# Kernel optimization log

Measured on AMD Instinct MI355X. Metric: run time of the kernel, lower is better.

## Reference

```python
import jax, jax.numpy as jnp
import numpy as np

N_NODES = 100000
N_EDGES = 1600000
N_FEAT = 128
HID = 64
HEADS = 3
CHROM = 21
N_CLASSES = 10
N_GRAPHS = 8
NEG_SLOPE = 0.2
EPS = 1e-5


def _glorot(key, shape):
    fan_in, fan_out = shape[0], shape[-1]
    lim = float(np.sqrt(6.0 / (fan_in + fan_out)))
    return jax.random.uniform(key, shape, jnp.float32, -lim, lim)


def setup_inputs() -> dict:
    key = jax.random.key(0)
    ks = jax.random.split(key, 16)
    x = jax.random.normal(ks[0], (N_NODES, N_FEAT), jnp.float32)
    src = jax.random.randint(ks[1], (N_EDGES,), 0, N_NODES)
    dst = jax.random.randint(ks[2], (N_EDGES,), 0, N_NODES)
    # avoid pre-existing self loops (PyG removes them before adding fresh ones)
    dst = jnp.where(dst == src, (dst + 1) % N_NODES, dst)
    edge_index = jnp.stack([src, dst]).astype(jnp.int64)
    batch = jnp.sort(jax.random.randint(ks[3], (N_NODES,), 0, N_GRAPHS)).astype(jnp.int64)
    d1 = HEADS * HID
    params = {
        # conv1: in 128 -> heads*64, concat=True
        'Wl1': _glorot(ks[4], (N_FEAT, d1)), 'Wr1': _glorot(ks[5], (N_FEAT, d1)),
        'att1': _glorot(ks[6], (HEADS, HID)), 'b1': jnp.zeros((d1,), jnp.float32),
        # batchnorm over 192 features
        'gamma': jnp.ones((d1,), jnp.float32), 'beta': jnp.zeros((d1,), jnp.float32),
        # conv2: in 192 -> 64 (mean over heads)
        'Wl2': _glorot(ks[7], (d1, d1)), 'Wr2': _glorot(ks[8], (d1, d1)),
        'att2': _glorot(ks[9], (HEADS, HID)), 'b2': jnp.zeros((HID,), jnp.float32),
        # conv3: in 64 -> 21 (mean over heads)
        'Wl3': _glorot(ks[10], (HID, HEADS * CHROM)), 'Wr3': _glorot(ks[11], (HID, HEADS * CHROM)),
        'att3': _glorot(ks[12], (HEADS, CHROM)), 'b3': jnp.zeros((CHROM,), jnp.float32),
        # classifier (sized to actual conv2 output width = HID)
        'Wc': _glorot(ks[13], (HID, N_CLASSES)), 'bc': jnp.zeros((N_CLASSES,), jnp.float32),
    }
    return {'x': x, 'edge_index': edge_index, 'batch': batch, **params}


def gatv2(x, src, dst, Wl, Wr, att, bias, concat):
    N = x.shape[0]
    H, D = att.shape
    xl = (x @ Wl).reshape(N, H, D)   # source transform (messages)
    xr = (x @ Wr).reshape(N, H, D)   # target transform
    e = jax.nn.leaky_relu(xl[src] + xr[dst], NEG_SLOPE)          # [E,H,D]
    logits = jnp.einsum('ehd,hd->eh', e, att)                    # [E,H]
    m = jax.ops.segment_max(logits, dst, num_segments=N)         # segment softmax over incoming edges
    ez = jnp.exp(logits - m[dst])
    z = jax.ops.segment_sum(ez, dst, num_segments=N)
    alpha = ez / z[dst]                                          # [E,H]; self-loops guarantee nonempty segments
    out = jax.ops.segment_sum(xl[src] * alpha[:, :, None], dst, num_segments=N)  # [N,H,D]
    out = out.reshape(N, H * D) if concat else out.mean(axis=1)
    return out + bias


def batchnorm(x, gamma, beta):
    mu = x.mean(axis=0)
    var = x.var(axis=0)
    return (x - mu) * jax.lax.rsqrt(var + EPS) * gamma + beta


def reference(x, edge_index, batch, Wl1, Wr1, att1, b1, gamma, beta,
              Wl2, Wr2, att2, b2, Wl3, Wr3, att3, b3, Wc, bc):
    N = x.shape[0]
    loop = jnp.arange(N, dtype=edge_index.dtype)
    src = jnp.concatenate([edge_index[0], loop])
    dst = jnp.concatenate([edge_index[1], loop])

    h = gatv2(x, src, dst, Wl1, Wr1, att1, b1, concat=True)      # [N, 192]
    h = jax.nn.relu(h)
    h = batchnorm(h, gamma, beta)
    h = gatv2(h, src, dst, Wl2, Wr2, att2, b2, concat=False)     # [N, 64]
    color = jax.nn.relu(h)
    color = gatv2(color, src, dst, Wl3, Wr3, att3, b3, concat=False)  # [N, 21]

    # global mean pool over graphs (dropout is eval-mode identity)
    sums = jax.ops.segment_sum(h, batch, num_segments=N_GRAPHS)
    cnt = jax.ops.segment_sum(jnp.ones((N, 1), h.dtype), batch, num_segments=N_GRAPHS)
    pooled = sums / jnp.maximum(cnt, 1.0)                        # [8, 64]
    classif = pooled @ Wc + bc                                   # [8, 10]
    return classif, color
```

## Files before the change

kernel.cpp:

```cpp
#include <hip/hip_runtime.h>
#include <stdint.h>
#include <math.h>

#define N_NODES 100000
#define N_EDGES 1600000
#define ETOT (N_EDGES + N_NODES)
#define NCLS 10
#define NGR 8
#define SCAN_BLOCKS ((N_NODES + 255) / 256)

typedef short v8s __attribute__((ext_vector_type(8)));
typedef float v4f __attribute__((ext_vector_type(4)));
typedef float f4v __attribute__((ext_vector_type(4)));
typedef unsigned short ushort_t;
typedef unsigned short us8 __attribute__((ext_vector_type(8)));
typedef unsigned short us4 __attribute__((ext_vector_type(4)));
typedef _Float16 h2 __attribute__((ext_vector_type(2)));
typedef _Float16 h4 __attribute__((ext_vector_type(4)));
typedef _Float16 h8 __attribute__((ext_vector_type(8)));

__device__ __forceinline__ float b2f(ushort_t u) {
    union { unsigned int i; float f; } v; v.i = ((unsigned int)u) << 16; return v.f;
}
__device__ __forceinline__ ushort_t f2b(float f) {
    union { float f; unsigned int i; } v; v.f = f;
    unsigned int u = v.i;
    unsigned int r = (u + 0x7fffu + ((u >> 16) & 1u)) >> 16;
    return (ushort_t)r;
}
__device__ __forceinline__ ushort_t f2h(float f) {
    union { _Float16 h; ushort_t u; } v; v.h = (_Float16)f; return v.u;
}

#if __has_builtin(__builtin_amdgcn_fdot2)
#define FDOT2(a, b, c) __builtin_amdgcn_fdot2((a), (b), (c), false)
#else
#define FDOT2(a, b, c) ((c) + (float)(a)[0] * (float)(b)[0] + (float)(a)[1] * (float)(b)[1])
#endif
#define SHUF2(v, i, j) __builtin_shufflevector((v), (v), (i), (j))

__device__ __forceinline__ h2 lrelu2(h2 t) {
    const h2 k = {(_Float16)0.2f, (_Float16)0.2f};
    return __builtin_elementwise_max(t, t * k);
}

__global__ void detect_kernel(const int* eidx, const unsigned int* gamma_raw,
                              int* nz, int* isf32) {
    int i = blockIdx.x * 256 + threadIdx.x;
    if (i == 0) *isf32 = (gamma_raw[0] == 0x3F800000u) ? 1 : 0;
    if (eidx[2 * i + 1] != 0) atomicAdd(nz, 1);
}

struct CArgs {
    const void* src[10];
    ushort_t*   dst[10];
    int         len[10];
    int         tohalf[10];
};
__global__ void convert_small(CArgs c, const int* isf32) {
    int seg = blockIdx.x;
    int f32 = *isf32;
    int th = c.tohalf[seg];
    for (int i = threadIdx.x; i < c.len[seg]; i += 256) {
        float v = f32 ? ((const float*)c.src[seg])[i] : b2f(((const ushort_t*)c.src[seg])[i]);
        c.dst[seg][i] = th ? f2h(v) : f2b(v);
    }
}

struct TArgs {
    const void* W[6];
    ushort_t*   Wt[6];
    int K[6], Nn[6], Kp[6], Np[6];
    int bstart[7];
};
__global__ void transpose_all(TArgs t, const int* isf32) {
    int b = blockIdx.x;
    int seg = 0;
    while (seg < 5 && b >= t.bstart[seg + 1]) seg++;
    int i = (b - t.bstart[seg]) * 256 + threadIdx.x;
    int Kp = t.Kp[seg];
    if (i >= t.Np[seg] * Kp) return;
    int n = i / Kp, k = i - n * Kp;
    ushort_t v = 0;
    if (n < t.Nn[seg] && k < t.K[seg]) {
        long idx = (long)k * t.Nn[seg] + n;
        v = (*isf32) ? f2b(((const float*)t.W[seg])[idx]) : ((const ushort_t*)t.W[seg])[idx];
    }
    t.Wt[seg][i] = v;
}

__global__ void hist_kernel(const int* eidx, const int* nz, int* counts) {
    long i = (long)blockIdx.x * 256 + threadIdx.x;
    if (i >= ETOT) return;
    int w64 = (*nz == 0);
    int d;
    if (i < N_EDGES) d = w64 ? eidx[2 * (N_EDGES + i)] : eidx[N_EDGES + i];
    else             d = (int)(i - N_EDGES);
    if ((unsigned)d >= N_NODES) d = 0;
    atomicAdd(&counts[d], 1);
}

__global__ void scan_part(const int* counts, int* blocksum) {
    __shared__ int red[256];
    int i = blockIdx.x * 256 + threadIdx.x;
    int v = (i < N_NODES) ? counts[i] : 0;
    red[threadIdx.x] = v;
    __syncthreads();
    for (int off = 128; off > 0; off >>= 1) {
        if (threadIdx.x < off) red[threadIdx.x] += red[threadIdx.x + off];
        __syncthreads();
    }
    if (threadIdx.x == 0) blocksum[blockIdx.x] = red[0];
}

__global__ void scan_top(int* blocksum) {
    __shared__ int part[512];
    int t = threadIdx.x;
    int v = (t < SCAN_BLOCKS) ? blocksum[t] : 0;
    part[t] = v;
    __syncthreads();
    for (int off = 1; off < 512; off <<= 1) {
        int x = part[t];
        int add = (t >= off) ? part[t - off] : 0;
        __syncthreads();
        part[t] = x + add;
        __syncthreads();
    }
    if (t < SCAN_BLOCKS) blocksum[t] = part[t] - v;
}

__global__ void scan_final(const int* counts, const int* blocksum, int* row_ptr) {
    __shared__ int part[256];
    int i = blockIdx.x * 256 + threadIdx.x;
    int v = (i < N_NODES) ? counts[i] : 0;
    part[threadIdx.x] = v;
    __syncthreads();
    for (int off = 1; off < 256; off <<= 1) {
        int x = part[threadIdx.x];
        int add = (threadIdx.x >= off) ? part[threadIdx.x - off] : 0;
        __syncthreads();
        part[threadIdx.x] = x + add;
        __syncthreads();
    }
    int incl = part[threadIdx.x];
    int base = blocksum[blockIdx.x];
    if (i < N_NODES) row_ptr[i] = base + incl - v;
    if (i == N_NODES - 1) row_ptr[N_NODES] = base + incl;
}

__global__ void scatter_kernel(const int* eidx, const int* nz, const int* row_ptr,
                               int* cursor, int* csr) {
    long i = (long)blockIdx.x * 256 + threadIdx.x;
    if (i >= ETOT) return;
    int w64 = (*nz == 0);
    int s, d;
    if (i < N_EDGES) {
        s = w64 ? eidx[2 * i] : eidx[i];
        d = w64 ? eidx[2 * (N_EDGES + i)] : eidx[N_EDGES + i];
    } else { s = d = (int)(i - N_EDGES); }
    if ((unsigned)s >= N_NODES) s = 0;
    if ((unsigned)d >= N_NODES) d = 0;
    int pos = atomicAdd(&cursor[d], 1);
    csr[row_ptr[d] + pos] = s;
}

template <int K, int MODE>
__global__ void gemm_dual_pack(const void* A, const short* W1t, const short* W2t,
                               ushort_t* O1A, ushort_t* O1B, ushort_t* O2A, ushort_t* O2B,
                               int srcauto, const float* scale, const float* shift,
                               const int* isf32) {
    constexpr int KITERS = K / 32;
    constexpr int NTILES = MODE ? 12 : 4;
    __shared__ ushort_t atile[32 * K];
    int tid = threadIdx.x;
    int f32src = srcauto && (*isf32);
    constexpr int CPR = K / 8;
    size_t nodeBase = (size_t)blockIdx.x * 32;

    for (int c = tid; c < 32 * CPR; c += 256) {
        int row = c / CPR, kc = c - row * CPR;
        size_t node = nodeBase + row;
        ushort_t tmp[8];
        if (f32src) {
            const f4v* src = (const f4v*)((const float*)A + node * K + kc * 8);
            f4v v0 = src[0], v1 = src[1];
            #pragma unroll
            for (int j = 0; j < 4; j++) { tmp[j] = f2b(v0[j]); tmp[4 + j] = f2b(v1[j]); }
        } else {
            us8 v = *(const us8*)((const ushort_t*)A + node * K + kc * 8);
            #pragma unroll
            for (int j = 0; j < 8; j++) tmp[j] = v[j];
        }
        if (scale) {
            #pragma unroll
            for (int j = 0; j < 8; j++)
                tmp[j] = f2b(b2f(tmp[j]) * scale[kc * 8 + j] + shift[kc * 8 + j]);
        }
        int ki = kc >> 2, q = kc & 3;
        *(us8*)&atile[((ki * 32 + row) * 4 + q) * 8] = *(us8*)tmp;
    }
    __syncthreads();

    int wave = tid >> 6, lane = tid & 63;
    int rw = lane & 15, q = lane >> 4;

    v8s afr[2][KITERS];
    #pragma unroll
    for (int m = 0; m < 2; m++)
        #pragma unroll
        for (int ki = 0; ki < KITERS; ki++)
            afr[m][ki] = *(const v8s*)&atile[((ki * 32 + m * 16 + rw) * 4 + q) * 8];

    for (int nt = wave; nt < NTILES; nt += 4) {
        const short* b1p = W1t + (size_t)(nt * 16 + rw) * K + q * 8;
        const short* b2p = W2t + (size_t)(nt * 16 + rw) * K + q * 8;
        v4f c1[2] = {{0,0,0,0},{0,0,0,0}}, c2[2] = {{0,0,0,0},{0,0,0,0}};
        #pragma unroll
        for (int ki = 0; ki < KITERS; ki++) {
            v8s b1 = *(const v8s*)(b1p + ki * 32);
            v8s b2 = *(const v8s*)(b2p + ki * 32);
            c1[0] = __builtin_amdgcn_mfma_f32_16x16x32_bf16(afr[0][ki], b1, c1[0], 0, 0, 0);
            c1[1] = __builtin_amdgcn_mfma_f32_16x16x32_bf16(afr[1][ki], b1, c1[1], 0, 0, 0);
            c2[0] = __builtin_amdgcn_mfma_f32_16x16x32_bf16(afr[0][ki], b2, c2[0], 0, 0, 0);
            c2[1] = __builtin_amdgcn_mfma_f32_16x16x32_bf16(afr[1][ki], b2, c2[1], 0, 0, 0);
        }
        int cn = nt * 16 + rw;
        #pragma unroll
        for (int m = 0; m < 2; m++) {
            if (MODE) {
                int h = cn >> 6, d = cn & 63;
                int l = d >> 2, k = d & 3;
                #pragma unroll
                for (int r = 0; r < 4; r++) {
                    size_t node = nodeBase + m * 16 + q * 4 + r;
                    if (h < 2) {
                        size_t ad = (node * 16 + l) * 8 + h * 4 + k;
                        O1A[ad] = f2h(c1[m][r]); O2A[ad] = f2h(c2[m][r]);
                    } else {
                        size_t ad = (node * 16 + l) * 4 + k;
                        O1B[ad] = f2h(c1[m][r]); O2B[ad] = f2h(c2[m][r]);
                    }
                }
            } else if (cn < 63) {
                int l = cn >> 2, k = cn & 3;
                #pragma unroll
                for (int r = 0; r < 4; r++) {
                    size_t node = nodeBase + m * 16 + q * 4 + r;
                    size_t ad = (node * 16 + l) * 4 + k;
                    O1A[ad] = f2h(c1[m][r]); O2A[ad] = f2h(c2[m][r]);
                }
            }
        }
    }
}

__global__ void edge_fused_192(const ushort_t* __restrict__ xlA_, const ushort_t* __restrict__ xlB_,
                               const ushort_t* __restrict__ xrA_, const ushort_t* __restrict__ xrB_,
                               const ushort_t* __restrict__ att_, const int* __restrict__ row_ptr,
                               const int* __restrict__ csr, const ushort_t* bias, int mode,
                               ushort_t* out_a, ushort_t* out_b) {
    const _Float16* xlA = (const _Float16*)xlA_;
    const _Float16* xlB = (const _Float16*)xlB_;
    const _Float16* xrA = (const _Float16*)xrA_;
    const _Float16* xrB = (const _Float16*)xrB_;
    const _Float16* att = (const _Float16*)att_;
    int wid = blockIdx.x * 4 + (threadIdx.x >> 6);
    int lane = threadIdx.x & 63;
    size_t n = wid;
    int quad = lane >> 4, l = lane & 15;

    h8 rv8 = *(const h8*)(xrA + (n * 16 + l) * 8);
    h4 rv4 = *(const h4*)(xrB + (n * 16 + l) * 4);
    h4 av0 = *(const h4*)(att + 4 * l);
    h4 av1 = *(const h4*)(att + 64 + 4 * l);
    h4 av2 = *(const h4*)(att + 128 + 4 * l);
    h2 rp0 = SHUF2(rv8, 0, 1), rp1 = SHUF2(rv8, 2, 3);
    h2 rp2 = SHUF2(rv8, 4, 5), rp3 = SHUF2(rv8, 6, 7);
    h2 rp4 = SHUF2(rv4, 0, 1), rp5 = SHUF2(rv4, 2, 3);
    h2 ap0 = SHUF2(av0, 0, 1), ap1 = SHUF2(av0, 2, 3);
    h2 ap2 = SHUF2(av1, 0, 1), ap3 = SHUF2(av1, 2, 3);
    h2 ap4 = SHUF2(av2, 0, 1), ap5 = SHUF2(av2, 2, 3);

    float z0 = 0.f, z1 = 0.f, z2 = 0.f;
    float A[12];
    #pragma unroll
    for (int k = 0; k < 12; k++) A[k] = 0.f;

    int beg = row_ptr[n], end = row_ptr[n + 1];
    for (int chunk = beg; chunk < end; chunk += 64) {
        int cnt = end - chunk; if (cnt > 64) cnt = 64;
        int sv = csr[chunk + (lane < cnt ? lane : cnt - 1)];
        for (int jj = 0; jj < cnt; jj += 4) {
            int j = jj + quad;
            int act = j < cnt;
            int jc = act ? j : cnt - 1;
            size_t s = (size_t)__shfl(sv, jc, 64);
            h8 xv8 = *(const h8*)(xlA + (s * 16 + l) * 8);
            h4 xv4 = *(const h4*)(xlB + (s * 16 + l) * 4);
            float p0 = FDOT2(ap0, lrelu2(SHUF2(xv8, 0, 1) + rp0), 0.f);
            p0 = FDOT2(ap1, lrelu2(SHUF2(xv8, 2, 3) + rp1), p0);
            float p1 = FDOT2(ap2, lrelu2(SHUF2(xv8, 4, 5) + rp2), 0.f);
            p1 = FDOT2(ap3, lrelu2(SHUF2(xv8, 6, 7) + rp3), p1);
            float p2 = FDOT2(ap4, lrelu2(SHUF2(xv4, 0, 1) + rp4), 0.f);
            p2 = FDOT2(ap5, lrelu2(SHUF2(xv4, 2, 3) + rp5), p2);
            #pragma unroll
            for (int o = 8; o > 0; o >>= 1) {
                p0 += __shfl_xor(p0, o, 64);
                p1 += __shfl_xor(p1, o, 64);
                p2 += __shfl_xor(p2, o, 64);
            }
            float e0 = act ? __expf(p0) : 0.f;
            float e1 = act ? __expf(p1) : 0.f;
            float e2 = act ? __expf(p2) : 0.f;
            z0 += e0; z1 += e1; z2 += e2;
            #pragma unroll
            for (int k = 0; k < 4; k++) {
                A[k]     = fmaf((float)xv8[k],     e0, A[k]);
                A[4 + k] = fmaf((float)xv8[4 + k], e1, A[4 + k]);
                A[8 + k] = fmaf((float)xv4[k],     e2, A[8 + k]);
            }
        }
    }

    #pragma unroll
    for (int st = 16; st <= 32; st <<= 1) {
        z0 += __shfl_xor(z0, st, 64);
        z1 += __shfl_xor(z1, st, 64);
        z2 += __shfl_xor(z2, st, 64);
        #pragma unroll
        for (int k = 0; k < 12; k++) A[k] += __shfl_xor(A[k], st, 64);
    }

    if (quad == 0) {
        float i0 = 1.f / z0, i1 = 1.f / z1, i2 = 1.f / z2;
        if (mode == 1) {
            ushort_t o0[4], o1[4], o2[4];
            #pragma unroll
            for (int k = 0; k < 4; k++) {
                o0[k] = f2b(fmaxf(A[k] * i0 + b2f(bias[4 * l + k]), 0.f));
                o1[k] = f2b(fmaxf(A[4 + k] * i1 + b2f(bias[64 + 4 * l + k]), 0.f));
                o2[k] = f2b(fmaxf(A[8 + k] * i2 + b2f(bias[128 + 4 * l + k]), 0.f));
            }
            *(uint2*)(out_a + n * 192 + 4 * l) = *(uint2*)o0;
            *(uint2*)(out_a + n * 192 + 64 + 4 * l) = *(uint2*)o1;
            *(uint2*)(out_a + n * 192 + 128 + 4 * l) = *(uint2*)o2;
        } else {
            ushort_t oh[4], oc[4];
            #pragma unroll
            for (int k = 0; k < 4; k++) {
                float hv = (A[k] * i0 + A[4 + k] * i1 + A[8 + k] * i2) * (1.0f / 3.0f)
                           + b2f(bias[4 * l + k]);
                oh[k] = f2b(hv);
                oc[k] = f2b(fmaxf(hv, 0.f));
            }
            *(uint2*)(out_a + n * 64 + 4 * l) = *(uint2*)oh;
            *(uint2*)(out_b + n * 64 + 4 * l) = *(uint2*)oc;
        }
    }
}

__global__ void edge_fused_63(const ushort_t* __restrict__ xl_, const ushort_t* __restrict__ xr_,
                              const ushort_t* __restrict__ att_, const int* __restrict__ row_ptr,
                              const int* __restrict__ csr, const ushort_t* bias,
                              void* dout, const int* isf32) {
    const _Float16* xl = (const _Float16*)xl_;
    const _Float16* xr = (const _Float16*)xr_;
    const _Float16* att = (const _Float16*)att_;
    __shared__ float ls[4 * 64];
    int wave = threadIdx.x >> 6;
    int wid = blockIdx.x * 4 + wave;
    int lane = threadIdx.x & 63;
    size_t n = wid;
    int quad = lane >> 4, l = lane & 15;
    int f0 = 4 * l;

    h2 ah[3][2];
    #pragma unroll
    for (int h = 0; h < 3; h++)
        #pragma unroll
        for (int p = 0; p < 2; p++) {
            int fa = f0 + 2 * p, fb = fa + 1;
            ah[h][p][0] = (fa < 63 && fa / 21 == h) ? att[fa] : (_Float16)0.f;
            ah[h][p][1] = (fb < 63 && fb / 21 == h) ? att[fb] : (_Float16)0.f;
        }
    bool b21[4], b42[4];
    #pragma unroll
    for (int k = 0; k < 4; k++) { b21[k] = (f0 + k) < 21; b42[k] = (f0 + k) < 42; }

    h4 rv = *(const h4*)(xr + (n * 16 + l) * 4);
    h2 r01 = SHUF2(rv, 0, 1), r23 = SHUF2(rv, 2, 3);

    float z0 = 0.f, z1 = 0.f, z2 = 0.f;
    float A[4] = {0.f, 0.f, 0.f, 0.f};

    int beg = row_ptr[n], end = row_ptr[n + 1];
    for (int chunk = beg; chunk < end; chunk += 64) {
        int cnt = end - chunk; if (cnt > 64) cnt = 64;
        int sv = csr[chunk + (lane < cnt ? lane : cnt - 1)];
        for (int jj = 0; jj < cnt; jj += 4) {
            int j = jj + quad;
            int act = j < cnt;
            int jc = act ? j : cnt - 1;
            size_t s = (size_t)__shfl(sv, jc, 64);
            h4 xv = *(const h4*)(xl + (s * 16 + l) * 4);
            h2 x01 = SHUF2(xv, 0, 1), x23 = SHUF2(xv, 2, 3);
            h2 t01 = lrelu2(x01 + r01), t23 = lrelu2(x23 + r23);
            float p0 = FDOT2(ah[0][1], t23, FDOT2(ah[0][0], t01, 0.f));
            float p1 = FDOT2(ah[1][1], t23, FDOT2(ah[1][0], t01, 0.f));
            float p2 = FDOT2(ah[2][1], t23, FDOT2(ah[2][0], t01, 0.f));
            #pragma unroll
            for (int o = 8; o > 0; o >>= 1) {
                p0 += __shfl_xor(p0, o, 64);
                p1 += __shfl_xor(p1, o, 64);
                p2 += __shfl_xor(p2, o, 64);
            }
            float e0 = act ? __expf(p0) : 0.f;
            float e1 = act ? __expf(p1) : 0.f;
            float e2 = act ? __expf(p2) : 0.f;
            z0 += e0; z1 += e1; z2 += e2;
            #pragma unroll
            for (int k = 0; k < 4; k++) {
                float ek = b21[k] ? e0 : (b42[k] ? e1 : e2);
                A[k] = fmaf((float)xv[k], ek, A[k]);
            }
        }
    }

    #pragma unroll
    for (int st = 16; st <= 32; st <<= 1) {
        z0 += __shfl_xor(z0, st, 64);
        z1 += __shfl_xor(z1, st, 64);
        z2 += __shfl_xor(z2, st, 64);
        #pragma unroll
        for (int k = 0; k < 4; k++) A[k] += __shfl_xor(A[k], st, 64);
    }

    if (quad == 0) {
        float i0 = 1.f / z0, i1 = 1.f / z1, i2 = 1.f / z2;
        #pragma unroll
        for (int k = 0; k < 4; k++) {
            float iv = b21[k] ? i0 : (b42[k] ? i1 : i2);
            ls[wave * 64 + f0 + k] = A[k] * iv;
        }
    }
    __syncthreads();
    if (lane < 21) {
        float o = (ls[wave * 64 + lane] + ls[wave * 64 + 21 + lane]
                   + ls[wave * 64 + 42 + lane]) * (1.0f / 3.0f) + b2f(bias[lane]);
        size_t oi = 80 + n * 21 + lane;
        if (*isf32) ((float*)dout)[oi] = o;
        else        ((ushort_t*)dout)[oi] = f2b(o);
    }
}

__global__ void bn_stats(const ushort_t* h, float* sum, float* sq) {
    int j = threadIdx.x;
    long r0 = (long)blockIdx.x * 256;
    float s = 0.f, q = 0.f;
    for (int i = 0; i < 256; i++) {
        long r = r0 + i;
        if (r >= N_NODES) break;
        float v = b2f(h[r * 192 + j]);
        s += v; q += v * v;
    }
    atomicAdd(&sum[j], s); atomicAdd(&sq[j], q);
}

__global__ void bn_finalize(const float* sum, const float* sq, const ushort_t* gamma,
                            const ushort_t* beta, float* scale, float* shift) {
    int j = threadIdx.x;
    if (j >= 192) return;
    float mu = sum[j] / (float)N_NODES;
    float var = sq[j] / (float)N_NODES - mu * mu;
    float inv = rsqrtf(fmaxf(var, 0.f) + 1e-5f);
    float sc = b2f(gamma[j]) * inv;
    scale[j] = sc;
    shift[j] = b2f(beta[j]) - mu * sc;
}

__global__ void pool_accum(const ushort_t* h2, const int* batchp, const int* nz,
                           float* psum, float* pcnt) {
    __shared__ float ls[NGR * 64];
    __shared__ float lc[NGR];
    for (int i = threadIdx.x; i < NGR * 64; i += blockDim.x) ls[i] = 0.f;
    if (threadIdx.x < NGR) lc[threadIdx.x] = 0.f;
    __syncthreads();
    int w64 = (*nz == 0);
    int f = threadIdx.x & 63;
    int rr = threadIdx.x >> 6;
    long r0 = (long)blockIdx.x * 1024;
    long rend = r0 + 1024; if (rend > N_NODES) rend = N_NODES;
    for (long r = r0 + rr; r < rend; r += 4) {
        int g = w64 ? batchp[2 * r] : batchp[r];
        g &= 7;
        atomicAdd(&ls[g * 64 + f], b2f(h2[r * 64 + f]));
        if (f == 0) atomicAdd(&lc[g], 1.0f);
    }
    __syncthreads();
    for (int i = threadIdx.x; i < NGR * 64; i += blockDim.x) atomicAdd(&psum[i], ls[i]);
    if (threadIdx.x < NGR) atomicAdd(&pcnt[threadIdx.x], lc[threadIdx.x]);
}

__global__ void classifier(const float* psum, const float* pcnt, const ushort_t* Wc,
                           const ushort_t* bc, void* dout, const int* isf32) {
    int i = threadIdx.x;
    if (i >= NGR * NCLS) return;
    int g = i / NCLS, c = i - g * NCLS;
    float cnt = fmaxf(pcnt[g], 1.0f);
    float s = 0.f;
    for (int d = 0; d < 64; d++)
        s += (psum[g * 64 + d] / cnt) * b2f(Wc[d * NCLS + c]);
    float o = s + b2f(bc[c]);
    if (*isf32) ((float*)dout)[i] = o;
    else        ((ushort_t*)dout)[i] = f2b(o);
}

extern "C" void kernel_launch(void* const* d_in, const int* in_sizes, int n_in,
                              void* d_out, int out_size, void* d_ws, size_t ws_size,
                              hipStream_t stream) {
    const void* x_raw   = d_in[0];
    const int*  eidx    = (const int*)d_in[1];
    const int*  batch   = (const int*)d_in[2];
    const void* Wl1     = d_in[3];
    const void* Wr1     = d_in[4];
    const void* att1r   = d_in[5];
    const void* b1r     = d_in[6];
    const void* gammar  = d_in[7];
    const void* betar   = d_in[8];
    const void* Wl2     = d_in[9];
    const void* Wr2     = d_in[10];
    const void* att2r   = d_in[11];
    const void* b2r     = d_in[12];
    const void* Wl3     = d_in[13];
    const void* Wr3     = d_in[14];
    const void* att3r   = d_in[15];
    const void* b3r     = d_in[16];
    const void* Wcr     = d_in[17];
    const void* bcr     = d_in[18];

    char* w = (char*)d_ws;
    size_t off = 0;
    auto alloc = [&](size_t bytes) -> char* {
        char* p = w + off;
        off = (off + bytes + 255) & ~(size_t)255;
        return p;
    };

    size_t meta_beg = off;
    int*   nz      = (int*)alloc(4);
    int*   isf32   = (int*)alloc(4);
    int*   counts  = (int*)alloc(4 * (size_t)N_NODES);
    int*   cursor  = (int*)alloc(4 * (size_t)N_NODES);
    float* bn_sum  = (float*)alloc(4 * 192);
    float* bn_sq   = (float*)alloc(4 * 192);
    float* psum    = (float*)alloc(4 * NGR * 64);
    float* pcnt    = (float*)alloc(4 * NGR);
    size_t meta_bytes = off - meta_beg;

    float* bn_scale = (float*)alloc(4 * 192);
    float* bn_shift = (float*)alloc(4 * 192);
    int*   blocksum = (int*)alloc(4 * 512);
    int*   row_ptr  = (int*)alloc(4 * (size_t)(N_NODES + 1));
    int*   csr      = (int*)alloc(4 * (size_t)ETOT);
    ushort_t* xlpA  = (ushort_t*)alloc(2 * (size_t)N_NODES * 128);
    ushort_t* xrpA  = (ushort_t*)alloc(2 * (size_t)N_NODES * 128);
    ushort_t* xlpB  = (ushort_t*)alloc(2 * (size_t)N_NODES * 64);
    ushort_t* xrpB  = (ushort_t*)alloc(2 * (size_t)N_NODES * 64);
    ushort_t* regC  = (ushort_t*)alloc(2 * (size_t)N_NODES * 192);
    ushort_t* hbn    = regC;
    ushort_t* h2v    = regC;
    ushort_t* colorb = regC + (size_t)N_NODES * 64;
    ushort_t* wt1l  = (ushort_t*)alloc(2 * 192 * 128);
    ushort_t* wt1r  = (ushort_t*)alloc(2 * 192 * 128);
    ushort_t* wt2l  = (ushort_t*)alloc(2 * 192 * 192);
    ushort_t* wt2r  = (ushort_t*)alloc(2 * 192 * 192);
    ushort_t* wt3l  = (ushort_t*)alloc(2 * 64 * 64);
    ushort_t* wt3r  = (ushort_t*)alloc(2 * 64 * 64);
    ushort_t* att1c = (ushort_t*)alloc(2 * 192);
    ushort_t* att2c = (ushort_t*)alloc(2 * 192);
    ushort_t* att3c = (ushort_t*)alloc(2 * 64);
    ushort_t* b1c   = (ushort_t*)alloc(2 * 192);
    ushort_t* b2c   = (ushort_t*)alloc(2 * 64);
    ushort_t* b3c   = (ushort_t*)alloc(2 * 32);
    ushort_t* gamc  = (ushort_t*)alloc(2 * 192);
    ushort_t* betc  = (ushort_t*)alloc(2 * 192);
    ushort_t* Wcc   = (ushort_t*)alloc(2 * 640);
    ushort_t* bcc   = (ushort_t*)alloc(2 * 16);
    (void)ws_size; (void)in_sizes; (void)n_in; (void)out_size;

    hipMemsetAsync(w + meta_beg, 0, meta_bytes, stream);

    detect_kernel<<<256, 256, 0, stream>>>(eidx, (const unsigned int*)gammar, nz, isf32);

    {
        CArgs c;
        const void* s[10] = {att1r, att2r, att3r, b1r, b2r, b3r, gammar, betar, Wcr, bcr};
        ushort_t* d[10]   = {att1c, att2c, att3c, b1c, b2c, b3c, gamc,  betc,  Wcc, bcc};
        int ln[10]        = {192,   192,   63,    192, 64,  21,  192,   192,   640, 10};
        int th[10]        = {1,     1,     1,     0,   0,   0,   0,     0,     0,   0};
        for (int i = 0; i < 10; i++) {
            c.src[i] = s[i]; c.dst[i] = d[i]; c.len[i] = ln[i]; c.tohalf[i] = th[i];
        }
        convert_small<<<10, 256, 0, stream>>>(c, isf32);
    }

    {
        TArgs t;
        const void* s[6] = {Wl1, Wr1, Wl2, Wr2, Wl3, Wr3};
        ushort_t* d[6]   = {wt1l, wt1r, wt2l, wt2r, wt3l, wt3r};
        int K[6]  = {128, 128, 192, 192, 64, 64};
        int Nn[6] = {192, 192, 192, 192, 63, 63};
        int Kp[6] = {128, 128, 192, 192, 64, 64};
        int Np[6] = {192, 192, 192, 192, 64, 64};
        int bs = 0;
        for (int i = 0; i < 6; i++) {
            t.W[i] = s[i]; t.Wt[i] = d[i];
            t.K[i] = K[i]; t.Nn[i] = Nn[i]; t.Kp[i] = Kp[i]; t.Np[i] = Np[i];
            t.bstart[i] = bs;
            bs += (Np[i] * Kp[i] + 255) / 256;
        }
        t.bstart[6] = bs;
        transpose_all<<<bs, 256, 0, stream>>>(t, isf32);
    }

    hist_kernel<<<(ETOT + 255) / 256, 256, 0, stream>>>(eidx, nz, counts);
    scan_part<<<SCAN_BLOCKS, 256, 0, stream>>>(counts, blocksum);
    scan_top<<<1, 512, 0, stream>>>(blocksum);
    scan_final<<<SCAN_BLOCKS, 256, 0, stream>>>(counts, blocksum, row_ptr);
    scatter_kernel<<<(ETOT + 255) / 256, 256, 0, stream>>>(eidx, nz, row_ptr, cursor, csr);

    const int nodeBlocks = N_NODES / 4;
    const int gemmBlocks = N_NODES / 32;

    gemm_dual_pack<128, 1><<<gemmBlocks, 256, 0, stream>>>(
        x_raw, (const short*)wt1l, (const short*)wt1r,
        xlpA, xlpB, xrpA, xrpB, 1, nullptr, nullptr, isf32);
    edge_fused_192<<<nodeBlocks, 256, 0, stream>>>(xlpA, xlpB, xrpA, xrpB, att1c,
                                                   row_ptr, csr, b1c, 1, hbn, hbn);

    bn_stats<<<(N_NODES + 255) / 256, 192, 0, stream>>>(hbn, bn_sum, bn_sq);
    bn_finalize<<<1, 192, 0, stream>>>(bn_sum, bn_sq, gamc, betc, bn_scale, bn_shift);

    gemm_dual_pack<192, 1><<<gemmBlocks, 256, 0, stream>>>(
        hbn, (const short*)wt2l, (const short*)wt2r,
        xlpA, xlpB, xrpA, xrpB, 0, bn_scale, bn_shift, isf32);
    edge_fused_192<<<nodeBlocks, 256, 0, stream>>>(xlpA, xlpB, xrpA, xrpB, att2c,
                                                   row_ptr, csr, b2c, 2, h2v, colorb);

    pool_accum<<<(N_NODES + 1023) / 1024, 256, 0, stream>>>(h2v, batch, nz, psum, pcnt);

    gemm_dual_pack<64, 0><<<gemmBlocks, 256, 0, stream>>>(
        colorb, (const short*)wt3l, (const short*)wt3r,
        xlpA, xlpB, xrpA, xrpB, 0, nullptr, nullptr, isf32);
    edge_fused_63<<<nodeBlocks, 256, 0, stream>>>(xlpA, xrpA, att3c, row_ptr, csr,
                                                  b3c, d_out, isf32);

    classifier<<<1, 128, 0, stream>>>(psum, pcnt, Wcc, bcc, d_out, isf32);
}
```

Measured before the change: 947.0 us.

## Merge prep kernels, vectorize edge-index loads, add nontemporal hints, unroll BN stats

Merges the small-parameter conversion and weight-transpose kernels into one launch. The histogram and CSR scatter kernels now handle two edges per thread, reading edge indices with wider vector nontemporal loads. CSR reads in the edge kernels and CSR writes in scatter use nontemporal hints, and the BN statistics loop is unrolled by four. The goal is to cut launch overhead and memory traffic cost in graph construction, at the risk of nontemporal hints hurting cache reuse of csr in the later edge passes.

Measured after the change: 911.6 us. -3.7%, faster.

```diff
diff --git a/kernel.cpp b/kernel.cpp
--- a/kernel.cpp
+++ b/kernel.cpp
@@ -12,6 +12,8 @@
 typedef short v8s __attribute__((ext_vector_type(8)));
 typedef float v4f __attribute__((ext_vector_type(4)));
 typedef float f4v __attribute__((ext_vector_type(4)));
+typedef int i2v __attribute__((ext_vector_type(2)));
+typedef int i4v __attribute__((ext_vector_type(4)));
 typedef unsigned short ushort_t;
 typedef unsigned short us8 __attribute__((ext_vector_type(8)));
 typedef unsigned short us4 __attribute__((ext_vector_type(4)));
@@ -51,53 +53,63 @@
     if (eidx[2 * i + 1] != 0) atomicAdd(nz, 1);
 }
 
-struct CArgs {
-    const void* src[10];
-    ushort_t*   dst[10];
-    int         len[10];
-    int         tohalf[10];
-};
-__global__ void convert_small(CArgs c, const int* isf32) {
-    int seg = blockIdx.x;
-    int f32 = *isf32;
-    int th = c.tohalf[seg];
-    for (int i = threadIdx.x; i < c.len[seg]; i += 256) {
-        float v = f32 ? ((const float*)c.src[seg])[i] : b2f(((const ushort_t*)c.src[seg])[i]);
-        c.dst[seg][i] = th ? f2h(v) : f2b(v);
-    }
-}
-
-struct TArgs {
+struct PArgs {
+    const void* csrc[10];
+    ushort_t*   cdst[10];
+    int         clen[10];
+    int         cth[10];
     const void* W[6];
     ushort_t*   Wt[6];
     int K[6], Nn[6], Kp[6], Np[6];
-    int bstart[7];
+    int tb[7];
 };
-__global__ void transpose_all(TArgs t, const int* isf32) {
-    int b = blockIdx.x;
+__global__ void prep_kernel(PArgs a, const int* isf32) {
+    int f32 = *isf32;
+    if (blockIdx.x < 10) {
+        int seg = blockIdx.x;
+        int th = a.cth[seg];
+        for (int i = threadIdx.x; i < a.clen[seg]; i += 256) {
+            float v = f32 ? ((const float*)a.csrc[seg])[i]
+                          : b2f(((const ushort_t*)a.csrc[seg])[i]);
+            a.cdst[seg][i] = th ? f2h(v) : f2b(v);
+        }
+        return;
+    }
+    int b = blockIdx.x - 10;
     int seg = 0;
-    while (seg < 5 && b >= t.bstart[seg + 1]) seg++;
-    int i = (b - t.bstart[seg]) * 256 + threadIdx.x;
-    int Kp = t.Kp[seg];
-    if (i >= t.Np[seg] * Kp) return;
+    while (seg < 5 && b >= a.tb[seg + 1]) seg++;
+    int i = (b - a.tb[seg]) * 256 + threadIdx.x;
+    int Kp = a.Kp[seg];
+    if (i >= a.Np[seg] * Kp) return;
     int n = i / Kp, k = i - n * Kp;
     ushort_t v = 0;
-    if (n < t.Nn[seg] && k < t.K[seg]) {
-        long idx = (long)k * t.Nn[seg] + n;
-        v = (*isf32) ? f2b(((const float*)t.W[seg])[idx]) : ((const ushort_t*)t.W[seg])[idx];
-    }
-    t.Wt[seg][i] = v;
+    if (n < a.Nn[seg] && k < a.K[seg]) {
+        long idx = (long)k * a.Nn[seg] + n;
+        v = f32 ? f2b(((const float*)a.W[seg])[idx]) : ((const ushort_t*)a.W[seg])[idx];
+    }
+    a.Wt[seg][i] = v;
 }
 
 __global__ void hist_kernel(const int* eidx, const int* nz, int* counts) {
-    long i = (long)blockIdx.x * 256 + threadIdx.x;
-    if (i >= ETOT) return;
-    int w64 = (*nz == 0);
-    int d;
-    if (i < N_EDGES) d = w64 ? eidx[2 * (N_EDGES + i)] : eidx[N_EDGES + i];
-    else             d = (int)(i - N_EDGES);
-    if ((unsigned)d >= N_NODES) d = 0;
-    atomicAdd(&counts[d], 1);
+    long p = (long)blockIdx.x * 256 + threadIdx.x;
+    if (p >= ETOT / 2) return;
+    long e = 2 * p;
+    int d0, d1;
+    if (e < N_EDGES) {
+        if (*nz == 0) {
+            i4v v = __builtin_nontemporal_load(((const i4v*)(eidx + 2 * (size_t)N_EDGES)) + p);
+            d0 = v.x; d1 = v.z;
+        } else {
+            i2v v = __builtin_nontemporal_load(((const i2v*)(eidx + (size_t)N_EDGES)) + p);
+            d0 = v.x; d1 = v.y;
+        }
+    } else {
+        d0 = (int)(e - N_EDGES); d1 = d0 + 1;
+    }
+    if ((unsigned)d0 >= N_NODES) d0 = 0;
+    if ((unsigned)d1 >= N_NODES) d1 = 0;
+    atomicAdd(&counts[d0], 1);
+    atomicAdd(&counts[d1], 1);
 }
 
 __global__ void scan_part(const int* counts, int* blocksum) {
@@ -150,18 +162,31 @@
 
 __global__ void scatter_kernel(const int* eidx, const int* nz, const int* row_ptr,
                                int* cursor, int* csr) {
-    long i = (long)blockIdx.x * 256 + threadIdx.x;
-    if (i >= ETOT) return;
-    int w64 = (*nz == 0);
-    int s, d;
-    if (i < N_EDGES) {
-        s = w64 ? eidx[2 * i] : eidx[i];
-        d = w64 ? eidx[2 * (N_EDGES + i)] : eidx[N_EDGES + i];
-    } else { s = d = (int)(i - N_EDGES); }
-    if ((unsigned)s >= N_NODES) s = 0;
-    if ((unsigned)d >= N_NODES) d = 0;
-    int pos = atomicAdd(&cursor[d], 1);
-    csr[row_ptr[d] + pos] = s;
+    long p = (long)blockIdx.x * 256 + threadIdx.x;
+    if (p >= ETOT / 2) return;
+    long e = 2 * p;
+    int s0, s1, d0, d1;
+    if (e < N_EDGES) {
+        if (*nz == 0) {
+            i4v sv = __builtin_nontemporal_load(((const i4v*)eidx) + p);
+            i4v dv = __builtin_nontemporal_load(((const i4v*)(eidx + 2 * (size_t)N_EDGES)) + p);
+            s0 = sv.x; s1 = sv.z; d0 = dv.x; d1 = dv.z;
+        } else {
+            i2v sv = __builtin_nontemporal_load(((const i2v*)eidx) + p);
+            i2v dv = __builtin_nontemporal_load(((const i2v*)(eidx + (size_t)N_EDGES)) + p);
+            s0 = sv.x; s1 = sv.y; d0 = dv.x; d1 = dv.y;
+        }
+    } else {
+        s0 = d0 = (int)(e - N_EDGES); s1 = d1 = s0 + 1;
+    }
+    if ((unsigned)s0 >= N_NODES) s0 = 0;
+    if ((unsigned)d0 >= N_NODES) d0 = 0;
+    if ((unsigned)s1 >= N_NODES) s1 = 0;
+    if ((unsigned)d1 >= N_NODES) d1 = 0;
+    int pos0 = atomicAdd(&cursor[d0], 1);
+    __builtin_nontemporal_store(s0, &csr[row_ptr[d0] + pos0]);
+    int pos1 = atomicAdd(&cursor[d1], 1);
+    __builtin_nontemporal_store(s1, &csr[row_ptr[d1] + pos1]);
 }
 
 template <int K, int MODE>
@@ -289,7 +314,7 @@
     int beg = row_ptr[n], end = row_ptr[n + 1];
     for (int chunk = beg; chunk < end; chunk += 64) {
         int cnt = end - chunk; if (cnt > 64) cnt = 64;
-        int sv = csr[chunk + (lane < cnt ? lane : cnt - 1)];
+        int sv = __builtin_nontemporal_load(csr + chunk + (lane < cnt ? lane : cnt - 1));
         for (int jj = 0; jj < cnt; jj += 4) {
             int j = jj + quad;
             int act = j < cnt;
@@ -396,7 +421,7 @@
     int beg = row_ptr[n], end = row_ptr[n + 1];
     for (int chunk = beg; chunk < end; chunk += 64) {
         int cnt = end - chunk; if (cnt > 64) cnt = 64;
-        int sv = csr[chunk + (lane < cnt ? lane : cnt - 1)];
+        int sv = __builtin_nontemporal_load(csr + chunk + (lane < cnt ? lane : cnt - 1));
         for (int jj = 0; jj < cnt; jj += 4) {
             int j = jj + quad;
             int act = j < cnt;
@@ -456,13 +481,18 @@
 __global__ void bn_stats(const ushort_t* h, float* sum, float* sq) {
     int j = threadIdx.x;
     long r0 = (long)blockIdx.x * 256;
+    long rend = r0 + 256; if (rend > N_NODES) rend = N_NODES;
     float s = 0.f, q = 0.f;
-    for (int i = 0; i < 256; i++) {
-        long r = r0 + i;
-        if (r >= N_NODES) break;
-        float v = b2f(h[r * 192 + j]);
-        s += v; q += v * v;
-    }
+    long r = r0;
+    for (; r + 4 <= rend; r += 4) {
+        float v0 = b2f(h[(r + 0) * 192 + j]);
+        float v1 = b2f(h[(r + 1) * 192 + j]);
+        float v2 = b2f(h[(r + 2) * 192 + j]);
+        float v3 = b2f(h[(r + 3) * 192 + j]);
+        s += (v0 + v1) + (v2 + v3);
+        q += (v0 * v0 + v1 * v1) + (v2 * v2 + v3 * v3);
+    }
+    for (; r < rend; r++) { float v = b2f(h[r * 192 + j]); s += v; q += v * v; }
     atomicAdd(&sum[j], s); atomicAdd(&sq[j], q);
 }
 
@@ -593,19 +623,14 @@
     detect_kernel<<<256, 256, 0, stream>>>(eidx, (const unsigned int*)gammar, nz, isf32);
 
     {
-        CArgs c;
-        const void* s[10] = {att1r, att2r, att3r, b1r, b2r, b3r, gammar, betar, Wcr, bcr};
-        ushort_t* d[10]   = {att1c, att2c, att3c, b1c, b2c, b3c, gamc,  betc,  Wcc, bcc};
-        int ln[10]        = {192,   192,   63,    192, 64,  21,  192,   192,   640, 10};
-        int th[10]        = {1,     1,     1,     0,   0,   0,   0,     0,     0,   0};
+        PArgs a;
+        const void* cs[10] = {att1r, att2r, att3r, b1r, b2r, b3r, gammar, betar, Wcr, bcr};
+        ushort_t* cd[10]   = {att1c, att2c, att3c, b1c, b2c, b3c, gamc,  betc,  Wcc, bcc};
+        int cl[10]         = {192,   192,   63,    192, 64,  21,  192,   192,   640, 10};
+        int ct[10]         = {1,     1,     1,     0,   0,   0,   0,     0,     0,   0};
         for (int i = 0; i < 10; i++) {
-            c.src[i] = s[i]; c.dst[i] = d[i]; c.len[i] = ln[i]; c.tohalf[i] = th[i];
-        }
-        convert_small<<<10, 256, 0, stream>>>(c, isf32);
-    }
-
-    {
-        TArgs t;
+            a.csrc[i] = cs[i]; a.cdst[i] = cd[i]; a.clen[i] = cl[i]; a.cth[i] = ct[i];
+        }
         const void* s[6] = {Wl1, Wr1, Wl2, Wr2, Wl3, Wr3};
         ushort_t* d[6]   = {wt1l, wt1r, wt2l, wt2r, wt3l, wt3r};
         int K[6]  = {128, 128, 192, 192, 64, 64};
@@ -614,20 +639,20 @@
         int Np[6] = {192, 192, 192, 192, 64, 64};
         int bs = 0;
         for (int i = 0; i < 6; i++) {
-            t.W[i] = s[i]; t.Wt[i] = d[i];
-            t.K[i] = K[i]; t.Nn[i] = Nn[i]; t.Kp[i] = Kp[i]; t.Np[i] = Np[i];
-            t.bstart[i] = bs;
+            a.W[i] = s[i]; a.Wt[i] = d[i];
+            a.K[i] = K[i]; a.Nn[i] = Nn[i]; a.Kp[i] = Kp[i]; a.Np[i] = Np[i];
+            a.tb[i] = bs;
             bs += (Np[i] * Kp[i] + 255) / 256;
         }
-        t.bstart[6] = bs;
-        transpose_all<<<bs, 256, 0, stream>>>(t, isf32);
-    }
-
-    hist_kernel<<<(ETOT + 255) / 256, 256, 0, stream>>>(eidx, nz, counts);
+        a.tb[6] = bs;
+        prep_kernel<<<10 + bs, 256, 0, stream>>>(a, isf32);
+    }
+
+    hist_kernel<<<(ETOT / 2 + 255) / 256, 256, 0, stream>>>(eidx, nz, counts);
     scan_part<<<SCAN_BLOCKS, 256, 0, stream>>>(counts, blocksum);
     scan_top<<<1, 512, 0, stream>>>(blocksum);
     scan_final<<<SCAN_BLOCKS, 256, 0, stream>>>(counts, blocksum, row_ptr);
-    scatter_kernel<<<(ETOT + 255) / 256, 256, 0, stream>>>(eidx, nz, row_ptr, cursor, csr);
+    scatter_kernel<<<(ETOT / 2 + 255) / 256, 256, 0, stream>>>(eidx, nz, row_ptr, cursor, csr);
 
     const int nodeBlocks = N_NODES / 4;
     const int gemmBlocks = N_NODES / 32;
```
